# Kernel tuning notes

Hardware: AMD Instinct MI355X
Metric: run time of the kernel (lower is better)

## Reference

```python
import jax, jax.numpy as jnp
import numpy as np

N, E, C, B = 8192, 131072, 256, 64
BINS = 256
CENTERS = jnp.linspace(-6.0, 0.0, BINS)
GAMMA = 255.0 / 6.0  # 1/lengthscale, lengthscale = mean diff of centers = 6/255


def _silu(x):
    return x * jax.nn.sigmoid(x)


def _ln(x, g, b):
    m = x.mean(-1, keepdims=True)
    v = ((x - m) ** 2).mean(-1, keepdims=True)
    return (x - m) / jnp.sqrt(v + 1e-5) * g + b


def _bn(x, g, b):  # training-mode BatchNorm1d (biased var over batch dim)
    m = x.mean(0)
    v = ((x - m) ** 2).mean(0)
    return (x - m) / jnp.sqrt(v + 1e-5) * g + b


def setup_inputs() -> dict:
    key = jax.random.key(0)
    ks = list(jax.random.split(key, 60))
    it = iter(ks)

    def nrm(shape, s=0.05):
        return (jax.random.normal(next(it), shape, dtype=jnp.float32) * s)

    inp = {}
    inp['node'] = jax.random.normal(next(it), (N, 92), dtype=jnp.float32)
    inp['edge_index'] = jax.random.randint(next(it), (2, E), 0, N)
    inp['edge_attr'] = jax.random.normal(next(it), (E, 3), dtype=jnp.float32)
    inp['pdd'] = jax.random.normal(next(it), (N, 51), dtype=jnp.float32)
    inp['batch'] = jnp.sort(jax.random.randint(next(it), (N,), 0, B))
    # atom embedding: Linear(92,C) -> SiLU -> Linear(C,C)
    inp['atom_W1'] = nrm((92, C)); inp['atom_b1'] = jnp.zeros((C,), jnp.float32)
    inp['atom_W2'] = nrm((C, C)); inp['atom_b2'] = jnp.zeros((C,), jnp.float32)
    # edge embedding: RBF(256) -> Linear(256,C) -> SiLU
    inp['edge_W'] = nrm((BINS, C)); inp['edge_b'] = jnp.zeros((C,), jnp.float32)
    # pdd embedding: Linear(51,C)
    inp['pdd_W'] = nrm((51, C)); inp['pdd_b'] = jnp.zeros((C,), jnp.float32)
    # 3 PDDFormerConv layers (Matformer-style), stacked on leading dim
    inp['conv_Wq'] = nrm((3, C, C)); inp['conv_bq'] = jnp.zeros((3, C), jnp.float32)
    inp['conv_Wk'] = nrm((3, C, C)); inp['conv_bk'] = jnp.zeros((3, C), jnp.float32)
    inp['conv_Wv'] = nrm((3, C, C)); inp['conv_bv'] = jnp.zeros((3, C), jnp.float32)
    inp['conv_We'] = nrm((3, C, C)); inp['conv_be'] = jnp.zeros((3, C), jnp.float32)
    inp['conv_Wku'] = nrm((3, 3 * C, C)); inp['conv_bku'] = jnp.zeros((3, C), jnp.float32)
    inp['conv_Wmu'] = nrm((3, 3 * C, C)); inp['conv_bmu'] = jnp.zeros((3, C), jnp.float32)
    inp['conv_Wm'] = nrm((3, C, C)); inp['conv_bm'] = jnp.zeros((3, C), jnp.float32)
    inp['conv_ln_m_g'] = jnp.ones((3, C), jnp.float32); inp['conv_ln_m_b'] = jnp.zeros((3, C), jnp.float32)
    inp['conv_ln_a_g'] = jnp.ones((3, C), jnp.float32); inp['conv_ln_a_b'] = jnp.zeros((3, C), jnp.float32)
    inp['conv_bn_g'] = jnp.ones((3, C), jnp.float32); inp['conv_bn_b'] = jnp.zeros((3, C), jnp.float32)
    # 2 PDD_Conv layers
    inp['pddc_W1'] = nrm((2, C, 2 * C)); inp['pddc_b1'] = jnp.zeros((2, 2 * C), jnp.float32)
    inp['pddc_W2'] = nrm((2, C, C)); inp['pddc_b2'] = jnp.zeros((2, C), jnp.float32)
    inp['pddc_W3'] = nrm((2, C, C)); inp['pddc_b3'] = jnp.zeros((2, C), jnp.float32)
    inp['pddc_bn_g'] = jnp.ones((2, C), jnp.float32); inp['pddc_bn_b'] = jnp.zeros((2, C), jnp.float32)
    # head
    inp['fc_W'] = nrm((C, C)); inp['fc_b'] = jnp.zeros((C,), jnp.float32)
    inp['out_W'] = nrm((C, 1)); inp['out_b'] = jnp.zeros((1,), jnp.float32)
    return inp


def reference(node, edge_index, edge_attr, pdd, batch,
              atom_W1, atom_b1, atom_W2, atom_b2, edge_W, edge_b, pdd_W, pdd_b,
              conv_Wq, conv_bq, conv_Wk, conv_bk, conv_Wv, conv_bv, conv_We, conv_be,
              conv_Wku, conv_bku, conv_Wmu, conv_bmu, conv_Wm, conv_bm,
              conv_ln_m_g, conv_ln_m_b, conv_ln_a_g, conv_ln_a_b, conv_bn_g, conv_bn_b,
              pddc_W1, pddc_b1, pddc_W2, pddc_b2, pddc_W3, pddc_b3, pddc_bn_g, pddc_bn_b,
              fc_W, fc_b, out_W, out_b):
    src, dst = edge_index[0], edge_index[1]
    # embeddings
    x = _silu(node @ atom_W1 + atom_b1) @ atom_W2 + atom_b2            # [N,C]
    d = -1.0 / jnp.linalg.norm(edge_attr, axis=1)                      # [E]
    rbf = jnp.exp(-GAMMA * (d[:, None] - CENTERS) ** 2)                # [E,BINS]
    e_in = _silu(rbf @ edge_W + edge_b)                                # [E,C]
    p = pdd @ pdd_W + pdd_b                                            # [N,C]
    scale = 1.0 / jnp.sqrt(jnp.float32(C))

    def conv(x, i):
        q = x @ conv_Wq[i] + conv_bq[i]
        k = x @ conv_Wk[i] + conv_bk[i]
        v = x @ conv_Wv[i] + conv_bv[i]
        e = e_in @ conv_We[i] + conv_be[i]
        key_e = jnp.concatenate([k[dst], k[src], e], axis=-1) @ conv_Wku[i] + conv_bku[i]
        alpha = q[dst] * key_e * scale
        msg = jnp.concatenate([v[dst], v[src], e], axis=-1) @ conv_Wmu[i] + conv_bmu[i]
        msg = msg * jax.nn.sigmoid(_ln(alpha, conv_ln_a_g[i], conv_ln_a_b[i]))
        msg = _ln(msg @ conv_Wm[i] + conv_bm[i], conv_ln_m_g[i], conv_ln_m_b[i])
        agg = jax.ops.segment_sum(msg, dst, num_segments=N)
        return jax.nn.softplus(x + _bn(agg, conv_bn_g[i], conv_bn_b[i]))

    def pddc(x, adj, i):
        adj = adj + x
        a2 = _bn(adj, pddc_bn_g[i], pddc_bn_b[i]) @ pddc_W1[i] + pddc_b1[i]
        x1, x2 = a2[:, :C], a2[:, C:]
        x1 = x1 @ pddc_W2[i] + pddc_b2[i]
        x2 = jax.nn.gelu(x2, approximate=False)  # dropout inactive at eval
        return (x1 * x2) @ pddc_W3[i] + pddc_b3[i] + x, adj

    x = conv(x, 0)
    x, p = pddc(x, p, 0)
    x = conv(x, 1)
    x, p = pddc(x, p, 1)
    x = conv(x, 2)
    counts = jnp.maximum(jax.ops.segment_sum(jnp.ones((N,), x.dtype), batch, num_segments=B), 1.0)
    pooled = jax.ops.segment_sum(x, batch, num_segments=B) / counts[:, None]
    cf = pooled + _silu(pooled @ fc_W + fc_b)
    return jnp.squeeze(cf @ out_W + out_b)  # [B]
```

## Files before the change

kernel.cpp:

```cpp
#include <hip/hip_runtime.h>
#include <hip/hip_bf16.h>

#define Nn 8192
#define Ne 131072
#define Cc 256
#define Bb 64

typedef __hip_bfloat16 bf16;
typedef __attribute__((ext_vector_type(8))) short bf16x8;
typedef __attribute__((ext_vector_type(4))) float f32x4;

__device__ __forceinline__ float b2f(unsigned short s){
  return __uint_as_float(((unsigned)s) << 16);
}
__device__ __forceinline__ unsigned short f2b(float v){
  bf16 h = __float2bfloat16(v);
  return *(unsigned short*)&h;
}

__device__ __forceinline__ void block_reduce_2(float& s1, float& s2, float* sm){
#pragma unroll
  for (int off = 32; off > 0; off >>= 1){
    s1 += __shfl_down(s1, off, 64);
    s2 += __shfl_down(s2, off, 64);
  }
  int lane = threadIdx.x & 63;
  int wid  = threadIdx.x >> 6;
  if (lane == 0){ sm[wid] = s1; sm[4 + wid] = s2; }
  __syncthreads();
  s1 = sm[0] + sm[1] + sm[2] + sm[3];
  s2 = sm[4] + sm[5] + sm[6] + sm[7];
}

__global__ __launch_bounds__(256) void mg_k(
  const bf16* __restrict__ A,
  const bf16* __restrict__ Bpack, const float* __restrict__ bias,
  bf16* __restrict__ o0, bf16* __restrict__ o1, bf16* __restrict__ o2,
  bf16* __restrict__ o3, bf16* __restrict__ o4,
  float* __restrict__ fout, bf16* __restrict__ foutBf,
  int actMode, const int* __restrict__ outPerm)
{
  int lane = threadIdx.x & 63;
  int wave = threadIdx.x >> 6;
  int panel = blockIdx.x;
  long m0 = (long)blockIdx.y * 64;
  int row16 = lane & 15;
  int kg    = lane >> 4;

  const bf16* a0 = A + (m0 + row16) * 256 + kg * 8;
  const bf16* bp = Bpack + (size_t)panel * 65536;

  f32x4 acc[4][4];
#pragma unroll
  for (int i = 0; i < 4; i++)
#pragma unroll
    for (int j = 0; j < 4; j++) acc[i][j] = (f32x4){0.f, 0.f, 0.f, 0.f};

#pragma unroll
  for (int c8 = 0; c8 < 8; c8++){
    bf16x8 a[4], b[4];
#pragma unroll
    for (int im = 0; im < 4; im++)
      a[im] = *(const bf16x8*)(a0 + im * 4096 + c8 * 32);
#pragma unroll
    for (int in = 0; in < 4; in++)
      b[in] = *(const bf16x8*)(bp + ((size_t)((c8 * 16 + wave * 4 + in) * 64 + lane)) * 8);
#pragma unroll
    for (int im = 0; im < 4; im++)
#pragma unroll
      for (int in = 0; in < 4; in++)
        acc[im][in] = __builtin_amdgcn_mfma_f32_16x16x32_bf16(
                        a[im], b[in], acc[im][in], 0, 0, 0);
  }

  int colq = lane & 15;
  int quad = lane >> 4;

  if (fout){
#pragma unroll
    for (int im = 0; im < 4; im++)
#pragma unroll
      for (int in = 0; in < 4; in++){
        int col = wave * 64 + in * 16 + colq;
        float bv = bias ? bias[col] : 0.f;
#pragma unroll
        for (int r = 0; r < 4; r++){
          long row = m0 + im * 16 + quad * 4 + r;
          float v = acc[im][in][r] + bv + fout[row * 256 + col];
          fout[row * 256 + col] = v;
          if (foutBf) foutBf[row * 256 + col] = __float2bfloat16(v);
        }
      }
    return;
  }

  bf16* op = (panel == 0) ? o0 : (panel == 1) ? o1 : (panel == 2) ? o2
           : (panel == 3) ? o3 : o4;
#pragma unroll
  for (int im = 0; im < 4; im++){
    long orow[4];
#pragma unroll
    for (int r = 0; r < 4; r++){
      long row = m0 + im * 16 + quad * 4 + r;
      orow[r] = outPerm ? (long)outPerm[row] : row;
    }
#pragma unroll
    for (int in = 0; in < 4; in++){
      int col = wave * 64 + in * 16 + colq;
      float bv = bias ? bias[panel * 256 + col] : 0.f;
#pragma unroll
      for (int r = 0; r < 4; r++){
        float v = acc[im][in][r] + bv;
        if (actMode == 1) v = v / (1.f + __expf(-v));
        op[orow[r] * 256 + col] = __float2bfloat16(v);
      }
    }
  }
}

__global__ __launch_bounds__(256) void conv_edge_k(
  const bf16* __restrict__ e_in,
  const bf16* __restrict__ Bedge, const float* __restrict__ bedge,
  const bf16* __restrict__ Bm, const float* __restrict__ bm,
  const bf16* __restrict__ q,
  const bf16* __restrict__ kp1, const bf16* __restrict__ kp2,
  const bf16* __restrict__ vp1, const bf16* __restrict__ vp2,
  const int* __restrict__ dstS, const int* __restrict__ srcS,
  const float* __restrict__ lg, const float* __restrict__ lb,
  float* __restrict__ aggS)
{
  __shared__ bf16 eK[32 * 256];
  __shared__ bf16 eM[32 * 256];
  __shared__ int  sdst[32];
  int lane = threadIdx.x & 63;
  int wave = threadIdx.x >> 6;
  long m0 = (long)blockIdx.x * 32;
  int row16 = lane & 15;
  int kg    = lane >> 4;
  int colq  = row16;
  int quad  = kg;

  if (threadIdx.x < 32) sdst[threadIdx.x] = dstS[m0 + threadIdx.x];

  int drs[8], srs[8];
#pragma unroll
  for (int it = 0; it < 8; it++){
    drs[it] = dstS[m0 + it * 4 + wave];
    srs[it] = srcS[m0 + it * 4 + wave];
  }
  int c0g = lane * 4;
  ushort4 k1 = *(const ushort4*)((const unsigned short*)kp1 + (long)drs[0] * 256 + c0g);
  ushort4 k2 = *(const ushort4*)((const unsigned short*)kp2 + (long)srs[0] * 256 + c0g);
  ushort4 qv = *(const ushort4*)((const unsigned short*)q   + (long)drs[0] * 256 + c0g);
  ushort4 v1 = *(const ushort4*)((const unsigned short*)vp1 + (long)drs[0] * 256 + c0g);
  ushort4 v2 = *(const ushort4*)((const unsigned short*)vp2 + (long)srs[0] * 256 + c0g);

  const bf16* a0 = e_in + (m0 + row16) * 256 + kg * 8;

  for (int p = 0; p < 2; p++){
    const bf16* bp = Bedge + (size_t)p * 65536;
    f32x4 acc[2][4];
#pragma unroll
    for (int i = 0; i < 2; i++)
#pragma unroll
      for (int j = 0; j < 4; j++) acc[i][j] = (f32x4){0.f, 0.f, 0.f, 0.f};
#pragma unroll
    for (int c8 = 0; c8 < 8; c8++){
      bf16x8 a[2], b[4];
#pragma unroll
      for (int im = 0; im < 2; im++)
        a[im] = *(const bf16x8*)(a0 + im * 4096 + c8 * 32);
#pragma unroll
      for (int in = 0; in < 4; in++)
        b[in] = *(const bf16x8*)(bp + ((size_t)((c8 * 16 + wave * 4 + in) * 64 + lane)) * 8);
#pragma unroll
      for (int im = 0; im < 2; im++)
#pragma unroll
        for (int in = 0; in < 4; in++)
          acc[im][in] = __builtin_amdgcn_mfma_f32_16x16x32_bf16(
                          a[im], b[in], acc[im][in], 0, 0, 0);
    }
    bf16* E = p ? eM : eK;
    const float* bb = bedge + p * 256;
#pragma unroll
    for (int im = 0; im < 2; im++)
#pragma unroll
      for (int in = 0; in < 4; in++){
        int col = wave * 64 + in * 16 + colq;
        float bv = bb[col];
#pragma unroll
        for (int r = 0; r < 4; r++){
          int row = im * 16 + quad * 4 + r;
          int idx = row * 256 + ((((col >> 3) ^ (row & 7))) << 3) + (col & 7);
          E[idx] = __float2bfloat16(acc[im][in][r] + bv);
        }
      }
  }
  __syncthreads();

  {
    int cb = lane >> 1;
    int e0 = (lane & 1) * 4;
    float4 gv = *(const float4*)(lg + c0g);
    float4 bv = *(const float4*)(lb + c0g);
#pragma unroll
    for (int it = 0; it < 8; it++){
      int row = it * 4 + wave;
      int li = row * 256 + ((cb ^ (row & 7)) << 3) + e0;
      ushort4 ek = *(const ushort4*)((const unsigned short*)eK + li);
      ushort4 em = *(const ushort4*)((const unsigned short*)eM + li);
      ushort4 nk1, nk2, nqv, nv1, nv2;
      if (it < 7){
        long dr2 = drs[it + 1], sr2 = srs[it + 1];
        nk1 = *(const ushort4*)((const unsigned short*)kp1 + dr2 * 256 + c0g);
        nk2 = *(const ushort4*)((const unsigned short*)kp2 + sr2 * 256 + c0g);
        nqv = *(const ushort4*)((const unsigned short*)q   + dr2 * 256 + c0g);
        nv1 = *(const ushort4*)((const unsigned short*)vp1 + dr2 * 256 + c0g);
        nv2 = *(const ushort4*)((const unsigned short*)vp2 + sr2 * 256 + c0g);
      }
      float a0g = (b2f(ek.x) + b2f(k1.x) + b2f(k2.x)) * b2f(qv.x) * 0.0625f;
      float a1g = (b2f(ek.y) + b2f(k1.y) + b2f(k2.y)) * b2f(qv.y) * 0.0625f;
      float a2g = (b2f(ek.z) + b2f(k1.z) + b2f(k2.z)) * b2f(qv.z) * 0.0625f;
      float a3g = (b2f(ek.w) + b2f(k1.w) + b2f(k2.w)) * b2f(qv.w) * 0.0625f;
      float s1 = a0g + a1g + a2g + a3g;
      float s2 = a0g*a0g + a1g*a1g + a2g*a2g + a3g*a3g;
#pragma unroll
      for (int off = 1; off < 64; off <<= 1){
        s1 += __shfl_xor(s1, off, 64);
        s2 += __shfl_xor(s2, off, 64);
      }
      float mn  = s1 * (1.0f / Cc);
      float var = s2 * (1.0f / Cc) - mn * mn;
      float rs  = rsqrtf(var + 1e-5f);
      float g0 = 1.f / (1.f + __expf(-((a0g - mn) * rs * gv.x + bv.x)));
      float g1 = 1.f / (1.f + __expf(-((a1g - mn) * rs * gv.y + bv.y)));
      float g2 = 1.f / (1.f + __expf(-((a2g - mn) * rs * gv.z + bv.z)));
      float g3 = 1.f / (1.f + __expf(-((a3g - mn) * rs * gv.w + bv.w)));
      ushort4 o;
      o.x = f2b((b2f(em.x) + b2f(v1.x) + b2f(v2.x)) * g0);
      o.y = f2b((b2f(em.y) + b2f(v1.y) + b2f(v2.y)) * g1);
      o.z = f2b((b2f(em.z) + b2f(v1.z) + b2f(v2.z)) * g2);
      o.w = f2b((b2f(em.w) + b2f(v1.w) + b2f(v2.w)) * g3);
      *(ushort4*)((unsigned short*)eK + li) = o;
      k1 = nk1; k2 = nk2; qv = nqv; v1 = nv1; v2 = nv2;
    }
  }
  __syncthreads();

  f32x4 acc[2][4];
#pragma unroll
  for (int i = 0; i < 2; i++)
#pragma unroll
    for (int j = 0; j < 4; j++) acc[i][j] = (f32x4){0.f, 0.f, 0.f, 0.f};
  int r7 = row16 & 7;
#pragma unroll
  for (int c8 = 0; c8 < 8; c8++){
    bf16x8 a[2], b[4];
#pragma unroll
    for (int im = 0; im < 2; im++)
      a[im] = *(const bf16x8*)&eK[(row16 + im * 16) * 256 + (((c8 * 4 + kg) ^ r7) << 3)];
#pragma unroll
    for (int in = 0; in < 4; in++)
      b[in] = *(const bf16x8*)(Bm + ((size_t)((c8 * 16 + wave * 4 + in) * 64 + lane)) * 8);
#pragma unroll
    for (int im = 0; im < 2; im++)
#pragma unroll
      for (int in = 0; in < 4; in++)
        acc[im][in] = __builtin_amdgcn_mfma_f32_16x16x32_bf16(
                        a[im], b[in], acc[im][in], 0, 0, 0);
  }

  float s1a[2][4], s2a[2][4];
#pragma unroll
  for (int im = 0; im < 2; im++)
#pragma unroll
    for (int r = 0; r < 4; r++){
      float t1 = 0.f, t2 = 0.f;
#pragma unroll
      for (int in = 0; in < 4; in++){
        int col = wave * 64 + in * 16 + colq;
        float v = acc[im][in][r] + bm[col];
        t1 += v; t2 += v * v;
      }
#pragma unroll
      for (int off = 1; off < 16; off <<= 1){
        t1 += __shfl_xor(t1, off, 64);
        t2 += __shfl_xor(t2, off, 64);
      }
      s1a[im][r] = t1; s2a[im][r] = t2;
    }
  __syncthreads();
  float* red = (float*)eK;
  if (colq < 8){
    int imw = colq >> 2, rw = colq & 3;
    int rr = imw * 16 + quad * 4 + rw;
    red[(wave * 32 + rr) * 2 + 0] = s1a[imw][rw];
    red[(wave * 32 + rr) * 2 + 1] = s2a[imw][rw];
  }
  __syncthreads();
#pragma unroll
  for (int im = 0; im < 2; im++)
#pragma unroll
    for (int r = 0; r < 4; r++){
      int row = im * 16 + quad * 4 + r;
      float ts1 = red[row * 2]           + red[(32 + row) * 2]
                + red[(64 + row) * 2]    + red[(96 + row) * 2];
      float ts2 = red[row * 2 + 1]       + red[(32 + row) * 2 + 1]
                + red[(64 + row) * 2 + 1] + red[(96 + row) * 2 + 1];
      float mn  = ts1 * (1.0f / Cc);
      float var = ts2 * (1.0f / Cc) - mn * mn;
      float rs  = rsqrtf(var + 1e-5f);
#pragma unroll
      for (int in = 0; in < 4; in++){
        int col = wave * 64 + in * 16 + colq;
        float v = acc[im][in][r] + bm[col];
        ((unsigned short*)eM)[row * 256 + col] = f2b((v - mn) * rs);
      }
    }
  __syncthreads();

  {
    int t = threadIdx.x;
    float sum = 0.f;
    int cur = sdst[0];
    for (int r = 0; r < 32; r++){
      int d = sdst[r];
      if (d != cur){
        atomicAdd(&aggS[(long)cur * 256 + t], sum);
        sum = 0.f; cur = d;
      }
      sum += b2f(((const unsigned short*)eM)[r * 256 + t]);
    }
    atomicAdd(&aggS[(long)cur * 256 + t], sum);
  }
}

__global__ __launch_bounds__(256) void pack_b2_k(
  const float* __restrict__ W, int ldW, bf16* __restrict__ out)
{
  int panel = blockIdx.y;
  long p = (long)blockIdx.x * 256 + threadIdx.x;
  int j    = p & 7;
  int lane = (p >> 3) & 63;
  int nt   = (p >> 9) & 15;
  int kc   = p >> 13;
  int k = kc * 32 + (lane >> 4) * 8 + j;
  int n = nt * 16 + (lane & 15);
  out[(size_t)panel * 65536 + p] =
    __float2bfloat16(W[(long)k * ldW + panel * 256 + n]);
}

__global__ __launch_bounds__(256) void pack_qm_k(
  const float* __restrict__ Wq, const float* __restrict__ Wm,
  bf16* __restrict__ N5, bf16* __restrict__ WpM)
{
  int z = blockIdx.y;
  const float* W; bf16* out;
  if (z < 3){ W = Wq + (size_t)z * 65536; out = N5 + (size_t)z * 327680; }
  else      { W = Wm + (size_t)(z-3) * 65536; out = WpM + (size_t)(z-3) * 65536; }
  long p = (long)blockIdx.x * 256 + threadIdx.x;
  int j    = p & 7;
  int lane = (p >> 3) & 63;
  int nt   = (p >> 9) & 15;
  int kc   = p >> 13;
  int k = kc * 32 + (lane >> 4) * 8 + j;
  int n = nt * 16 + (lane & 15);
  out[p] = __float2bfloat16(W[(long)k * 256 + n]);
}

__global__ __launch_bounds__(256) void fold_k(
  const float* __restrict__ Wk, const float* __restrict__ Wv,
  const float* __restrict__ We,
  const float* __restrict__ Wku, const float* __restrict__ Wmu,
  bf16* __restrict__ N5, bf16* __restrict__ EG)
{
  int z = blockIdx.z, i = z / 6, j = z % 6;
  const float* A; const float* B; bf16* C;
  if (j < 2){
    A = Wk + (size_t)i * 65536; B = Wku + (size_t)i * 196608 + j * 65536;
    C = N5 + (size_t)i * 327680 + (size_t)(1 + j) * 65536;
  } else if (j < 4){
    A = Wv + (size_t)i * 65536; B = Wmu + (size_t)i * 196608 + (j - 2) * 65536;
    C = N5 + (size_t)i * 327680 + (size_t)(3 + (j - 2)) * 65536;
  } else {
    A = We + (size_t)i * 65536;
    B = (j == 4 ? Wku : Wmu) + (size_t)i * 196608 + 131072;
    C = EG + (size_t)i * 131072 + (size_t)(j - 4) * 65536;
  }

  __shared__ __align__(16) float As[16][64];
  __shared__ __align__(16) float Bs[16][128];
  int t = threadIdx.x;
  int m0 = blockIdx.x * 64;
  int n0 = blockIdx.y * 128;

  float acc[4][8];
#pragma unroll
  for (int a = 0; a < 4; a++)
#pragma unroll
    for (int b = 0; b < 8; b++) acc[a][b] = 0.f;
  int tm = t >> 4, tn = t & 15, mA = t & 63, kgA = t >> 6;

  for (int k0 = 0; k0 < 256; k0 += 16){
#pragma unroll
    for (int it = 0; it < 4; it++){
      int kl = kgA + it * 4;
      As[kl][mA] = A[(long)(m0 + mA) * 256 + k0 + kl];
    }
#pragma unroll
    for (int it = 0; it < 8; it++){
      int idx = t + it * 256;
      int kl = idx >> 7, n = idx & 127;
      Bs[kl][n] = B[(long)(k0 + kl) * 256 + n0 + n];
    }
    __syncthreads();
#pragma unroll
    for (int kk = 0; kk < 16; kk++){
      float4 a  = *(const float4*)&As[kk][tm * 4];
      float4 b0 = *(const float4*)&Bs[kk][tn * 4];
      float4 b1 = *(const float4*)&Bs[kk][64 + tn * 4];
      float av[4] = {a.x, a.y, a.z, a.w};
      float bv[8] = {b0.x, b0.y, b0.z, b0.w, b1.x, b1.y, b1.z, b1.w};
#pragma unroll
      for (int ii = 0; ii < 4; ii++)
#pragma unroll
        for (int jj = 0; jj < 8; jj++)
          acc[ii][jj] = __builtin_fmaf(av[ii], bv[jj], acc[ii][jj]);
    }
    __syncthreads();
  }
#pragma unroll
  for (int ii = 0; ii < 4; ii++){
    int m = m0 + tm * 4 + ii;
#pragma unroll
    for (int h = 0; h < 2; h++){
#pragma unroll
      for (int jj = 0; jj < 4; jj++){
        int n = n0 + h * 64 + tn * 4 + jj;
        int kc = m >> 5, nt = n >> 4;
        int ln_ = ((m >> 3) & 3) * 16 + (n & 15);
        long idx = ((long)(kc * 16 + nt) * 64 + ln_) * 8 + (m & 7);
        C[idx] = __float2bfloat16(acc[ii][h * 4 + jj]);
      }
    }
  }
}

__global__ __launch_bounds__(256) void gemm_k(
  const void* __restrict__ A0, int K0, int ld0,
  long M, int Nout,
  const float* __restrict__ W, const float* __restrict__ bias,
  const float* __restrict__ res, int ldRes,
  void* __restrict__ Cout, int outDt, int actMode)
{
  __shared__ __align__(16) float As[16][64];
  __shared__ __align__(16) float Bs[16][128];

  int t = threadIdx.x;
  long m0 = (long)blockIdx.x * 64;
  int  n0 = blockIdx.y * 128;

  float acc[4][8];
#pragma unroll
  for (int i = 0; i < 4; i++)
#pragma unroll
    for (int j = 0; j < 8; j++) acc[i][j] = 0.f;

  int tm = t >> 4, tn = t & 15, mA = t & 63, kgA = t >> 6;
  long rowA = m0 + mA;
  bool rv = rowA < M;

  for (int k0 = 0; k0 < K0; k0 += 16){
#pragma unroll
    for (int it = 0; it < 4; it++){
      int kl = kgA + it * 4;
      int k  = k0 + kl;
      float v = 0.f;
      if (rv && k < K0) v = ((const float*)A0)[rowA * (long)ld0 + k];
      As[kl][mA] = v;
    }
#pragma unroll
    for (int it = 0; it < 8; it++){
      int idx = t + it * 256;
      int kl = idx >> 7, n = idx & 127;
      int k  = k0 + kl;
      Bs[kl][n] = (k < K0) ? W[(long)k * Nout + n0 + n] : 0.f;
    }
    __syncthreads();
#pragma unroll
    for (int kk = 0; kk < 16; kk++){
      float4 a  = *(const float4*)&As[kk][tm * 4];
      float4 b0 = *(const float4*)&Bs[kk][tn * 4];
      float4 b1 = *(const float4*)&Bs[kk][64 + tn * 4];
      float av[4] = {a.x, a.y, a.z, a.w};
      float bv[8] = {b0.x, b0.y, b0.z, b0.w, b1.x, b1.y, b1.z, b1.w};
#pragma unroll
      for (int i = 0; i < 4; i++)
#pragma unroll
        for (int j = 0; j < 8; j++)
          acc[i][j] = __builtin_fmaf(av[i], bv[j], acc[i][j]);
    }
    __syncthreads();
  }

#pragma unroll
  for (int i = 0; i < 4; i++){
    long m = m0 + tm * 4 + i;
    if (m >= M) continue;
#pragma unroll
    for (int h = 0; h < 2; h++){
      int nb = n0 + h * 64 + tn * 4;
      float po[4];
#pragma unroll
      for (int j = 0; j < 4; j++){
        float v = acc[i][h * 4 + j];
        if (bias) v += bias[nb + j];
        if (actMode == 1) v = v / (1.0f + __expf(-v));
        if (res) v += res[m * (long)ldRes + nb + j];
        po[j] = v;
      }
      if (outDt){
        __align__(8) unsigned short tb[4];
#pragma unroll
        for (int j = 0; j < 4; j++) tb[j] = f2b(po[j]);
        *(short4*)((bf16*)Cout + m * (long)Nout + nb) = *(short4*)tb;
      } else {
        float4 ov = {po[0], po[1], po[2], po[3]};
        *(float4*)((float*)Cout + m * (long)Nout + nb) = ov;
      }
    }
  }
}

__global__ __launch_bounds__(256) void zero_k(float* __restrict__ p, long n){
  long i = (long)blockIdx.x * 256 + threadIdx.x;
  long stride = (long)gridDim.x * 256;
  for (; i < n; i += stride) p[i] = 0.f;
}
__global__ __launch_bounds__(256) void zero_i_k(int* __restrict__ p, long n){
  long i = (long)blockIdx.x * 256 + threadIdx.x;
  long stride = (long)gridDim.x * 256;
  for (; i < n; i += stride) p[i] = 0;
}
__global__ __launch_bounds__(256) void f2bf_k(bf16* __restrict__ d,
                                              const float* __restrict__ s, long n){
  long i = (long)blockIdx.x * 256 + threadIdx.x;
  long stride = (long)gridDim.x * 256;
  for (; i < n; i += stride) d[i] = __float2bfloat16(s[i]);
}

__global__ __launch_bounds__(256) void fuse_bias_all_k(
  const float* __restrict__ bku, const float* __restrict__ bmu,
  const float* __restrict__ be,
  const float* __restrict__ bk, const float* __restrict__ bv,
  const float* __restrict__ Wku, const float* __restrict__ Wmu,
  float* __restrict__ b_edge)
{
  int z = blockIdx.x, i = z >> 1, kind = z & 1;
  const float* W  = (kind ? Wmu : Wku) + (size_t)i * 196608;
  const float* b0 = (kind ? bmu : bku) + i * 256;
  const float* vb = (kind ? bv : bk) + i * 256;
  const float* eb = be + i * 256;
  int n = threadIdx.x;
  float s = b0[n];
  for (int k = 0; k < Cc; k++){
    s += eb[k] * W[(512 + k) * 256 + n];
    s += vb[k] * (W[k * 256 + n] + W[(256 + k) * 256 + n]);
  }
  b_edge[i * 512 + kind * 256 + n] = s;
}

__global__ __launch_bounds__(256) void nodeb_all_k(const float* __restrict__ bq,
                                                   float* __restrict__ out){
  int z = blockIdx.x, i = z / 5, p = z % 5;
  out[i * 1280 + p * 256 + threadIdx.x] = (p == 0) ? bq[i * 256 + threadIdx.x] : 0.f;
}

__global__ __launch_bounds__(256) void d_k(const float* __restrict__ ea,
                                           float* __restrict__ d, int E)
{
  int i = blockIdx.x * 256 + threadIdx.x;
  if (i < E){
    float a = ea[i * 3 + 0], b = ea[i * 3 + 1], c = ea[i * 3 + 2];
    d[i] = -rsqrtf(a * a + b * b + c * c);
  }
}

__global__ __launch_bounds__(256) void rbf_k(
  const float* __restrict__ d, bf16* __restrict__ out)
{
  long id = (long)blockIdx.x * 256 + threadIdx.x;
  long m = id >> 8;
  int  k = id & 255;
  float cen = -6.0f + (float)k * (6.0f / 255.0f);
  float df  = d[m] - cen;
  out[id] = __float2bfloat16(__expf(-42.5f * df * df));
}

__global__ __launch_bounds__(256) void hist_k(const int* __restrict__ dst,
                                              int* __restrict__ hist)
{
  int e = blockIdx.x * 256 + threadIdx.x;
  if (e < Ne) atomicAdd(&hist[dst[e]], 1);
}

__global__ __launch_bounds__(1024) void scan_k(
  const int* __restrict__ hist, int* __restrict__ rowptr, int* __restrict__ counter)
{
  __shared__ int part[1024];
  int t = threadIdx.x;
  int base = t * 8;
  int local[8];
  int s = 0;
#pragma unroll
  for (int i = 0; i < 8; i++){ local[i] = s; s += hist[base + i]; }
  part[t] = s;
  __syncthreads();
  for (int off = 1; off < 1024; off <<= 1){
    int v = (t >= off) ? part[t - off] : 0;
    __syncthreads();
    part[t] += v;
    __syncthreads();
  }
  int pre = (t == 0) ? 0 : part[t - 1];
#pragma unroll
  for (int i = 0; i < 8; i++){
    int rp = pre + local[i];
    rowptr[base + i] = rp;
    counter[base + i] = rp;
  }
  if (t == 1023) rowptr[8192] = part[1023];
}

__global__ __launch_bounds__(256) void perm_k(const int* __restrict__ dst,
                                              int* __restrict__ counter,
                                              int* __restrict__ pos)
{
  int e = blockIdx.x * 256 + threadIdx.x;
  if (e < Ne) pos[e] = atomicAdd(&counter[dst[e]], 1);
}

__global__ __launch_bounds__(256) void sortidx_k(
  const int* __restrict__ dst, const int* __restrict__ srcI,
  const int* __restrict__ pos, int* __restrict__ dstS, int* __restrict__ srcS)
{
  int e = blockIdx.x * 256 + threadIdx.x;
  if (e < Ne){
    int p = pos[e];
    dstS[p] = dst[e];
    srcS[p] = srcI[e];
  }
}

__global__ __launch_bounds__(256) void bn_stats_f(
  const float* __restrict__ S, const int* __restrict__ rowptr,
  const float* __restrict__ lg, const float* __restrict__ lb,
  float* __restrict__ sums)
{
  int c  = threadIdx.x;
  int r0 = blockIdx.x * 128;
  float gc = lg[c], bc = lb[c];
  float s1 = 0.f, s2 = 0.f;
  for (int r = r0; r < r0 + 128; r++){
    float cnt = (float)(rowptr[r + 1] - rowptr[r]);
    float y = gc * S[(long)r * Cc + c] + cnt * bc;
    s1 += y; s2 += y * y;
  }
  atomicAdd(&sums[c],      s1);
  atomicAdd(&sums[Cc + c], s2);
}

__global__ __launch_bounds__(256) void bn_apply_softplus_f(
  float* __restrict__ x, bf16* __restrict__ xbf,
  const float* __restrict__ S, const int* __restrict__ rowptr,
  const float* __restrict__ lg, const float* __restrict__ lb,
  const float* __restrict__ sums,
  const float* __restrict__ g, const float* __restrict__ b)
{
  long r = blockIdx.x;
  int c = threadIdx.x;
  float cnt = (float)(rowptr[r + 1] - rowptr[r]);
  float y = lg[c] * S[r * Cc + c] + cnt * lb[c];
  float m    = sums[c] * (1.0f / Nn);
  float var  = sums[Cc + c] * (1.0f / Nn) - m * m;
  float rstd = rsqrtf(var + 1e-5f);
  float bn = (y - m) * rstd * g[c] + b[c];
  float v  = x[r * Cc + c] + bn;
  float sp = (v > 0.f) ? v + log1pf(__expf(-v)) : log1pf(__expf(v));
  x[r * Cc + c] = sp;
  xbf[r * Cc + c] = __float2bfloat16(sp);
}

__global__ __launch_bounds__(256) void bn_stats_k(
  const float* __restrict__ X, int rows, float* __restrict__ sums)
{
  int c  = threadIdx.x;
  int r0 = blockIdx.x * 128;
  int re = r0 + 128; if (re > rows) re = rows;
  float s1 = 0.f, s2 = 0.f;
  for (int r = r0; r < re; r++){
    float v = X[(long)r * Cc + c];
    s1 += v; s2 += v * v;
  }
  atomicAdd(&sums[c],      s1);
  atomicAdd(&sums[Cc + c], s2);
}

__global__ __launch_bounds__(256) void bn_st_k(
  const float* __restrict__ sums, const float* __restrict__ g,
  const float* __restrict__ b, float* __restrict__ S, float* __restrict__ T)
{
  int c = threadIdx.x;
  float m    = sums[c] * (1.0f / Nn);
  float var  = sums[Cc + c] * (1.0f / Nn) - m * m;
  float rstd = rsqrtf(var + 1e-5f);
  S[c] = g[c] * rstd;
  T[c] = b[c] - m * rstd * g[c];
}

__global__ __launch_bounds__(256) void add_k(float* __restrict__ p,
                                             const float* __restrict__ x)
{
  long i = (long)blockIdx.x * 256 + threadIdx.x;
  p[i] += x[i];
}

__global__ __launch_bounds__(256) void bnaff_k(
  const float* __restrict__ p, const float* __restrict__ S,
  const float* __restrict__ T, bf16* __restrict__ out)
{
  long r = blockIdx.x;
  int c = threadIdx.x;
  out[r * 256 + c] = __float2bfloat16(p[r * 256 + c] * S[c] + T[c]);
}

__global__ __launch_bounds__(256) void mulgelu_bf_k(
  bf16* __restrict__ u, const bf16* __restrict__ x1,
  const bf16* __restrict__ a2b)
{
  long r = blockIdx.x;
  int c = threadIdx.x;
  float xg = b2f(*((const unsigned short*)a2b + r * 256 + c));
  float ge = 0.5f * xg * (1.0f + erff(xg * 0.70710678118654752f));
  float x1v = b2f(*((const unsigned short*)x1 + r * 256 + c));
  u[r * 256 + c] = __float2bfloat16(x1v * ge);
}

__global__ __launch_bounds__(256) void pool_k(
  const float* __restrict__ x, const int* __restrict__ batch,
  float* __restrict__ pooled, float* __restrict__ counts)
{
  long r = blockIdx.x;
  int c = threadIdx.x;
  long b = batch[r];
  atomicAdd(&pooled[b * Cc + c], x[r * Cc + c]);
  if (c == 0) atomicAdd(&counts[b], 1.0f);
}

__global__ __launch_bounds__(256) void pooldiv_k(
  float* __restrict__ pooled, const float* __restrict__ counts)
{
  int b = blockIdx.x;
  int c = threadIdx.x;
  float cnt = counts[b];
  if (cnt < 1.f) cnt = 1.f;
  pooled[b * Cc + c] /= cnt;
}

__global__ __launch_bounds__(256) void out_k(
  const float* __restrict__ cf, const float* __restrict__ ow,
  const float* __restrict__ ob, float* __restrict__ out)
{
  __shared__ float sm[8];
  int b = blockIdx.x;
  int c = threadIdx.x;
  float v = cf[(long)b * Cc + c] * ow[c];
  float dummy = 0.f;
  block_reduce_2(v, dummy, sm);
  if (c == 0) out[b] = v + ob[0];
}

static inline void launch_gemm(hipStream_t st,
  const void* A0, int K0, int ld0,
  long M, int Nout, const float* W, const float* bias,
  const float* res, int ldRes, void* Cout, int outDt, int act)
{
  dim3 grid((unsigned)((M + 63) / 64), (unsigned)(Nout / 128));
  gemm_k<<<grid, dim3(256), 0, st>>>(
    A0, K0, ld0, M, Nout, W, bias, res, ldRes, Cout, outDt, act);
}

static inline void launch_mg(hipStream_t st, long M, int panels,
  const bf16* A, const bf16* Bpack, const float* bias,
  bf16* o0, bf16* o1, bf16* o2, bf16* o3, bf16* o4,
  float* fout, bf16* foutBf, int act, const int* outPerm)
{
  dim3 grid((unsigned)panels, (unsigned)(M / 64));
  mg_k<<<grid, dim3(256), 0, st>>>(A, Bpack, bias, o0, o1, o2, o3, o4,
                                   fout, foutBf, act, outPerm);
}

extern "C" void kernel_launch(void* const* d_in, const int* in_sizes, int n_in,
                              void* d_out, int out_size, void* d_ws, size_t ws_size,
                              hipStream_t stream)
{
  (void)in_sizes; (void)n_in; (void)out_size; (void)ws_size;

  const float* node       = (const float*)d_in[0];
  const int*   edge_index = (const int*)  d_in[1];
  const float* edge_attr  = (const float*)d_in[2];
  const float* pdd        = (const float*)d_in[3];
  const int*   batch      = (const int*)  d_in[4];
  const float* atom_W1 = (const float*)d_in[5];
  const float* atom_b1 = (const float*)d_in[6];
  const float* atom_W2 = (const float*)d_in[7];
  const float* atom_b2 = (const float*)d_in[8];
  const float* edge_W  = (const float*)d_in[9];
  const float* edge_b  = (const float*)d_in[10];
  const float* pdd_W   = (const float*)d_in[11];
  const float* pdd_b   = (const float*)d_in[12];
  const float* conv_Wq = (const float*)d_in[13];
  const float* conv_bq = (const float*)d_in[14];
  const float* conv_Wk = (const float*)d_in[15];
  const float* conv_bk = (const float*)d_in[16];
  const float* conv_Wv = (const float*)d_in[17];
  const float* conv_bv = (const float*)d_in[18];
  const float* conv_We = (const float*)d_in[19];
  const float* conv_be = (const float*)d_in[20];
  const float* conv_Wku = (const float*)d_in[21];
  const float* conv_bku = (const float*)d_in[22];
  const float* conv_Wmu = (const float*)d_in[23];
  const float* conv_bmu = (const float*)d_in[24];
  const float* conv_Wm  = (const float*)d_in[25];
  const float* conv_bm  = (const float*)d_in[26];
  const float* ln_m_g = (const float*)d_in[27];
  const float* ln_m_b = (const float*)d_in[28];
  const float* ln_a_g = (const float*)d_in[29];
  const float* ln_a_b = (const float*)d_in[30];
  const float* bn_g   = (const float*)d_in[31];
  const float* bn_b   = (const float*)d_in[32];
  const float* pddc_W1 = (const float*)d_in[33];
  const float* pddc_b1 = (const float*)d_in[34];
  const float* pddc_W2 = (const float*)d_in[35];
  const float* pddc_b2 = (const float*)d_in[36];
  const float* pddc_W3 = (const float*)d_in[37];
  const float* pddc_b3 = (const float*)d_in[38];
  const float* pddc_bn_g = (const float*)d_in[39];
  const float* pddc_bn_b = (const float*)d_in[40];
  const float* fc_W  = (const float*)d_in[41];
  const float* fc_b  = (const float*)d_in[42];
  const float* out_W = (const float*)d_in[43];
  const float* out_b = (const float*)d_in[44];

  const int* src = edge_index;
  const int* dst = edge_index + Ne;

  char* ws = (char*)d_ws;
  size_t off = 0;
  auto alloc = [&](size_t nbytes) -> char* {
    char* ptr = ws + off;
    off += (nbytes + 255) & ~(size_t)255;
    return ptr;
  };
  bf16*  e_in = (bf16*) alloc((size_t)Ne * Cc * 2);
  bf16*  bufB = (bf16*) alloc((size_t)Ne * Cc * 2);
  bf16*  bufC = (bf16*) alloc((size_t)Ne * Cc * 2);
  float* x    = (float*)alloc((size_t)Nn * Cc * 4);
  float* p    = (float*)alloc((size_t)Nn * Cc * 4);
  float* agg  = (float*)alloc((size_t)Nn * Cc * 4);
  bf16*  x_bf  = (bf16*)alloc((size_t)Nn * Cc * 2);
  bf16*  q_bf  = (bf16*)alloc((size_t)Nn * Cc * 2);
  bf16*  kp1   = (bf16*)alloc((size_t)Nn * Cc * 2);
  bf16*  kp2   = (bf16*)alloc((size_t)Nn * Cc * 2);
  bf16*  vp1   = (bf16*)alloc((size_t)Nn * Cc * 2);
  bf16*  vp2   = (bf16*)alloc((size_t)Nn * Cc * 2);
  bf16*  WpN5  = (bf16*)alloc((size_t)3 * 5 * 65536 * 2);
  bf16*  WpEdge= (bf16*)alloc((size_t)3 * 2 * 65536 * 2);
  bf16*  WpM   = (bf16*)alloc((size_t)3 * 65536 * 2);
  bf16*  WpE   = (bf16*)alloc((size_t)65536 * 2);
  bf16*  WpP1  = (bf16*)alloc((size_t)2 * 2 * 65536 * 2);
  bf16*  WpP2  = (bf16*)alloc((size_t)2 * 65536 * 2);
  bf16*  WpP3  = (bf16*)alloc((size_t)2 * 65536 * 2);
  float* nodeb = (float*)alloc((size_t)3 * 1280 * 4);
  float* b_edge= (float*)alloc((size_t)3 * 512 * 4);
  int*   hist    = (int*)alloc((size_t)8192 * 4);
  int*   rowptr  = (int*)alloc((size_t)8193 * 4);
  int*   counter = (int*)alloc((size_t)8192 * 4);
  int*   pos     = (int*)alloc((size_t)Ne * 4);
  int*   dstS    = (int*)alloc((size_t)Ne * 4);
  int*   srcS    = (int*)alloc((size_t)Ne * 4);
  float* pooled = (float*)alloc((size_t)Bb * Cc * 4);
  float* counts = (float*)alloc((size_t)Bb * 4);
  float* cf     = (float*)alloc((size_t)Bb * Cc * 4);
  float* bnsum  = (float*)alloc(2 * Cc * 4);
  float* bnS    = (float*)alloc(Cc * 4);
  float* bnT    = (float*)alloc(Cc * 4);

  float* dArr   = (float*)bufC;
  float* hidden = (float*)(bufC + (size_t)1024 * 1024);
  bf16* a2a = bufC;
  bf16* a2b = bufC + (size_t)Nn * Cc;
  bf16* x1b = bufB;
  bf16* ub  = bufB + (size_t)Nn * Cc;

  zero_i_k<<<dim3(8), dim3(256), 0, stream>>>(hist, 8192);
  hist_k<<<dim3(Ne / 256), dim3(256), 0, stream>>>(dst, hist);
  scan_k<<<dim3(1), dim3(1024), 0, stream>>>(hist, rowptr, counter);
  perm_k<<<dim3(Ne / 256), dim3(256), 0, stream>>>(dst, counter, pos);
  sortidx_k<<<dim3(Ne / 256), dim3(256), 0, stream>>>(dst, src, pos, dstS, srcS);

  d_k<<<dim3((Ne + 255) / 256), dim3(256), 0, stream>>>(edge_attr, dArr, Ne);

  fold_k<<<dim3(4, 2, 18), dim3(256), 0, stream>>>(
    conv_Wk, conv_Wv, conv_We, conv_Wku, conv_Wmu, WpN5, WpEdge);
  pack_qm_k<<<dim3(256, 6), dim3(256), 0, stream>>>(conv_Wq, conv_Wm, WpN5, WpM);
  fuse_bias_all_k<<<dim3(6), dim3(256), 0, stream>>>(
    conv_bku, conv_bmu, conv_be, conv_bk, conv_bv, conv_Wku, conv_Wmu, b_edge);
  nodeb_all_k<<<dim3(15), dim3(256), 0, stream>>>(conv_bq, nodeb);
  pack_b2_k<<<dim3(256, 1), dim3(256), 0, stream>>>(edge_W, 256, WpE);
  for (int j = 0; j < 2; j++){
    pack_b2_k<<<dim3(256, 2), dim3(256), 0, stream>>>(
      pddc_W1 + (size_t)j * 256 * 512, 512, WpP1 + (size_t)j * 2 * 65536);
    pack_b2_k<<<dim3(256, 1), dim3(256), 0, stream>>>(
      pddc_W2 + (size_t)j * 65536, 256, WpP2 + (size_t)j * 65536);
    pack_b2_k<<<dim3(256, 1), dim3(256), 0, stream>>>(
      pddc_W3 + (size_t)j * 65536, 256, WpP3 + (size_t)j * 65536);
  }

  launch_gemm(stream, node, 92, 92, Nn, Cc, atom_W1, atom_b1,
              nullptr, 0, hidden, 0, 1);
  launch_gemm(stream, hidden, 256, 256, Nn, Cc, atom_W2, atom_b2,
              nullptr, 0, x, 0, 0);
  f2bf_k<<<dim3(512), dim3(256), 0, stream>>>(x_bf, x, (long)Nn * Cc);
  launch_gemm(stream, pdd, 51, 51, Nn, Cc, pdd_W, pdd_b,
              nullptr, 0, p, 0, 0);
  rbf_k<<<dim3(Ne), dim3(256), 0, stream>>>(dArr, bufB);
  launch_mg(stream, Ne, 1, bufB, WpE, edge_b,
            e_in, nullptr, nullptr, nullptr, nullptr, nullptr, nullptr, 1, pos);

  for (int i = 0; i < 3; i++){
    launch_mg(stream, Nn, 5, x_bf, WpN5 + (size_t)i * 5 * 65536, nodeb + i * 1280,
              q_bf, kp1, kp2, vp1, vp2, nullptr, nullptr, 0, nullptr);
    zero_k<<<dim3(1024), dim3(256), 0, stream>>>(agg, (long)Nn * Cc);
    conv_edge_k<<<dim3(Ne / 32), dim3(256), 0, stream>>>(
      e_in, WpEdge + (size_t)i * 2 * 65536, b_edge + i * 512,
      WpM + (size_t)i * 65536, conv_bm + i * 256,
      q_bf, kp1, kp2, vp1, vp2, dstS, srcS,
      ln_a_g + i * 256, ln_a_b + i * 256, agg);
    zero_k<<<dim3(2), dim3(256), 0, stream>>>(bnsum, 2 * Cc);
    bn_stats_f<<<dim3(Nn / 128), dim3(256), 0, stream>>>(agg, rowptr,
              ln_m_g + i * 256, ln_m_b + i * 256, bnsum);
    bn_apply_softplus_f<<<dim3(Nn), dim3(256), 0, stream>>>(x, x_bf, agg, rowptr,
              ln_m_g + i * 256, ln_m_b + i * 256, bnsum,
              bn_g + i * 256, bn_b + i * 256);

    if (i < 2){
      int j = i;
      add_k<<<dim3(Nn * Cc / 256), dim3(256), 0, stream>>>(p, x);
      zero_k<<<dim3(2), dim3(256), 0, stream>>>(bnsum, 2 * Cc);
      bn_stats_k<<<dim3(Nn / 128), dim3(256), 0, stream>>>(p, Nn, bnsum);
      bn_st_k<<<dim3(1), dim3(256), 0, stream>>>(bnsum,
              pddc_bn_g + j * 256, pddc_bn_b + j * 256, bnS, bnT);
      bnaff_k<<<dim3(Nn), dim3(256), 0, stream>>>(p, bnS, bnT, x_bf);
      launch_mg(stream, Nn, 2, x_bf, WpP1 + (size_t)j * 2 * 65536, pddc_b1 + j * 512,
                a2a, a2b, nullptr, nullptr, nullptr, nullptr, nullptr, 0, nullptr);
      launch_mg(stream, Nn, 1, a2a, WpP2 + (size_t)j * 65536, pddc_b2 + j * 256,
                x1b, nullptr, nullptr, nullptr, nullptr, nullptr, nullptr, 0, nullptr);
      mulgelu_bf_k<<<dim3(Nn), dim3(256), 0, stream>>>(ub, x1b, a2b);
      launch_mg(stream, Nn, 1, ub, WpP3 + (size_t)j * 65536, pddc_b3 + j * 256,
                nullptr, nullptr, nullptr, nullptr, nullptr, x, x_bf, 0, nullptr);
    }
  }

  zero_k<<<dim3(64), dim3(256), 0, stream>>>(pooled, (long)Bb * Cc);
  zero_k<<<dim3(1), dim3(256), 0, stream>>>(counts, Bb);
  pool_k<<<dim3(Nn), dim3(256), 0, stream>>>(x, batch, pooled, counts);
  pooldiv_k<<<dim3(Bb), dim3(256), 0, stream>>>(pooled, counts);
  launch_gemm(stream, pooled, 256, 256, Bb, Cc, fc_W, fc_b,
              pooled, Cc, cf, 0, 1);
  out_k<<<dim3(Bb), dim3(256), 0, stream>>>(cf, out_W, out_b, (float*)d_out);
}
```

Baseline: 1.614 ms.

## Fuse RBF into edge GEMM, GELU into GEMM epilogue, and merge small kernels

Computes the RBF expansion directly in registers inside a dedicated MFMA GEMM kernel, so the 131072x256 bf16 RBF matrix is no longer written to and read back from memory. It also fuses the GELU multiply into the pddc W2 GEMM epilogue, merges the residual add with the BN statistics pass, folds the BN scale/shift computation into the affine kernel, and combines several zeroing launches. The cost is recomputing exp in the GEMM A-operand path and per-element erf in the epilogue, plus extra global reads of the aux tensor inside the GEMM.

```diff
diff --git a/kernel.cpp b/kernel.cpp
--- a/kernel.cpp
+++ b/kernel.cpp
@@ -38,7 +38,8 @@
   bf16* __restrict__ o0, bf16* __restrict__ o1, bf16* __restrict__ o2,
   bf16* __restrict__ o3, bf16* __restrict__ o4,
   float* __restrict__ fout, bf16* __restrict__ foutBf,
-  int actMode, const int* __restrict__ outPerm)
+  int actMode, const int* __restrict__ outPerm,
+  const bf16* __restrict__ gelAux)
 {
   int lane = threadIdx.x & 63;
   int wave = threadIdx.x >> 6;
@@ -110,9 +111,83 @@
       float bv = bias ? bias[panel * 256 + col] : 0.f;
 #pragma unroll
       for (int r = 0; r < 4; r++){
+        long row = m0 + im * 16 + quad * 4 + r;
         float v = acc[im][in][r] + bv;
         if (actMode == 1) v = v / (1.f + __expf(-v));
+        if (gelAux){
+          float xg = b2f(((const unsigned short*)gelAux)[row * 256 + col]);
+          v *= 0.5f * xg * (1.0f + erff(xg * 0.70710678118654752f));
+        }
         op[orow[r] * 256 + col] = __float2bfloat16(v);
+      }
+    }
+  }
+}
+
+__global__ __launch_bounds__(256) void rbf_mg_k(
+  const float* __restrict__ dArr,
+  const bf16* __restrict__ Bpack, const float* __restrict__ bias,
+  bf16* __restrict__ out, const int* __restrict__ outPerm)
+{
+  int lane = threadIdx.x & 63;
+  int wave = threadIdx.x >> 6;
+  long m0 = (long)blockIdx.x * 64;
+  int row16 = lane & 15;
+  int kg    = lane >> 4;
+
+  float dv[4];
+#pragma unroll
+  for (int im = 0; im < 4; im++) dv[im] = dArr[m0 + row16 + im * 16];
+
+  f32x4 acc[4][4];
+#pragma unroll
+  for (int i = 0; i < 4; i++)
+#pragma unroll
+    for (int j = 0; j < 4; j++) acc[i][j] = (f32x4){0.f, 0.f, 0.f, 0.f};
+
+#pragma unroll
+  for (int c8 = 0; c8 < 8; c8++){
+    bf16x8 a[4], b[4];
+#pragma unroll
+    for (int im = 0; im < 4; im++){
+#pragma unroll
+      for (int j = 0; j < 8; j++){
+        int k = c8 * 32 + kg * 8 + j;
+        float cen = -6.0f + (float)k * (6.0f / 255.0f);
+        float df  = dv[im] - cen;
+        a[im][j] = (short)f2b(__expf(-42.5f * df * df));
+      }
+    }
+#pragma unroll
+    for (int in = 0; in < 4; in++)
+      b[in] = *(const bf16x8*)(Bpack + ((size_t)((c8 * 16 + wave * 4 + in) * 64 + lane)) * 8);
+#pragma unroll
+    for (int im = 0; im < 4; im++)
+#pragma unroll
+      for (int in = 0; in < 4; in++)
+        acc[im][in] = __builtin_amdgcn_mfma_f32_16x16x32_bf16(
+                        a[im], b[in], acc[im][in], 0, 0, 0);
+  }
+
+  int colq = lane & 15;
+  int quad = lane >> 4;
+#pragma unroll
+  for (int im = 0; im < 4; im++){
+    long orow[4];
+#pragma unroll
+    for (int r = 0; r < 4; r++){
+      long row = m0 + im * 16 + quad * 4 + r;
+      orow[r] = outPerm ? (long)outPerm[row] : row;
+    }
+#pragma unroll
+    for (int in = 0; in < 4; in++){
+      int col = wave * 64 + in * 16 + colq;
+      float bv = bias[col];
+#pragma unroll
+      for (int r = 0; r < 4; r++){
+        float v = acc[im][in][r] + bv;
+        v = v / (1.f + __expf(-v));
+        out[orow[r] * 256 + col] = __float2bfloat16(v);
       }
     }
   }
@@ -537,6 +612,13 @@
   long stride = (long)gridDim.x * 256;
   for (; i < n; i += stride) p[i] = 0.f;
 }
+__global__ __launch_bounds__(256) void zero2_k(float* __restrict__ a, long na,
+                                               float* __restrict__ b2, long nb){
+  long i = (long)blockIdx.x * 256 + threadIdx.x;
+  long stride = (long)gridDim.x * 256;
+  for (long j = i; j < na; j += stride) a[j] = 0.f;
+  for (long j = i; j < nb; j += stride) b2[j] = 0.f;
+}
 __global__ __launch_bounds__(256) void zero_i_k(int* __restrict__ p, long n){
   long i = (long)blockIdx.x * 256 + threadIdx.x;
   long stride = (long)gridDim.x * 256;
@@ -584,17 +666,6 @@
     float a = ea[i * 3 + 0], b = ea[i * 3 + 1], c = ea[i * 3 + 2];
     d[i] = -rsqrtf(a * a + b * b + c * c);
   }
-}
-
-__global__ __launch_bounds__(256) void rbf_k(
-  const float* __restrict__ d, bf16* __restrict__ out)
-{
-  long id = (long)blockIdx.x * 256 + threadIdx.x;
-  long m = id >> 8;
-  int  k = id & 255;
-  float cen = -6.0f + (float)k * (6.0f / 255.0f);
-  float df  = d[m] - cen;
-  out[id] = __float2bfloat16(__expf(-42.5f * df * df));
 }
 
 __global__ __launch_bounds__(256) void hist_k(const int* __restrict__ dst,
@@ -691,59 +762,34 @@
   xbf[r * Cc + c] = __float2bfloat16(sp);
 }
 
-__global__ __launch_bounds__(256) void bn_stats_k(
-  const float* __restrict__ X, int rows, float* __restrict__ sums)
+__global__ __launch_bounds__(256) void add_stats_k(
+  float* __restrict__ p, const float* __restrict__ x, float* __restrict__ sums)
 {
   int c  = threadIdx.x;
   int r0 = blockIdx.x * 128;
-  int re = r0 + 128; if (re > rows) re = rows;
   float s1 = 0.f, s2 = 0.f;
-  for (int r = r0; r < re; r++){
-    float v = X[(long)r * Cc + c];
+  for (int r = r0; r < r0 + 128; r++){
+    float v = p[(long)r * Cc + c] + x[(long)r * Cc + c];
+    p[(long)r * Cc + c] = v;
     s1 += v; s2 += v * v;
   }
   atomicAdd(&sums[c],      s1);
   atomicAdd(&sums[Cc + c], s2);
 }
 
-__global__ __launch_bounds__(256) void bn_st_k(
-  const float* __restrict__ sums, const float* __restrict__ g,
-  const float* __restrict__ b, float* __restrict__ S, float* __restrict__ T)
-{
+__global__ __launch_bounds__(256) void bnaff_st_k(
+  const float* __restrict__ p, const float* __restrict__ sums,
+  const float* __restrict__ g, const float* __restrict__ b,
+  bf16* __restrict__ out)
+{
+  long r = blockIdx.x;
   int c = threadIdx.x;
   float m    = sums[c] * (1.0f / Nn);
   float var  = sums[Cc + c] * (1.0f / Nn) - m * m;
   float rstd = rsqrtf(var + 1e-5f);
-  S[c] = g[c] * rstd;
-  T[c] = b[c] - m * rstd * g[c];
-}
-
-__global__ __launch_bounds__(256) void add_k(float* __restrict__ p,
-                                             const float* __restrict__ x)
-{
-  long i = (long)blockIdx.x * 256 + threadIdx.x;
-  p[i] += x[i];
-}
-
-__global__ __launch_bounds__(256) void bnaff_k(
-  const float* __restrict__ p, const float* __restrict__ S,
-  const float* __restrict__ T, bf16* __restrict__ out)
-{
-  long r = blockIdx.x;
-  int c = threadIdx.x;
-  out[r * 256 + c] = __float2bfloat16(p[r * 256 + c] * S[c] + T[c]);
-}
-
-__global__ __launch_bounds__(256) void mulgelu_bf_k(
-  bf16* __restrict__ u, const bf16* __restrict__ x1,
-  const bf16* __restrict__ a2b)
-{
-  long r = blockIdx.x;
-  int c = threadIdx.x;
-  float xg = b2f(*((const unsigned short*)a2b + r * 256 + c));
-  float ge = 0.5f * xg * (1.0f + erff(xg * 0.70710678118654752f));
-  float x1v = b2f(*((const unsigned short*)x1 + r * 256 + c));
-  u[r * 256 + c] = __float2bfloat16(x1v * ge);
+  float S = g[c] * rstd;
+  float T = b[c] - m * rstd * g[c];
+  out[r * 256 + c] = __float2bfloat16(p[r * 256 + c] * S + T);
 }
 
 __global__ __launch_bounds__(256) void pool_k(
@@ -793,11 +839,12 @@
 static inline void launch_mg(hipStream_t st, long M, int panels,
   const bf16* A, const bf16* Bpack, const float* bias,
   bf16* o0, bf16* o1, bf16* o2, bf16* o3, bf16* o4,
-  float* fout, bf16* foutBf, int act, const int* outPerm)
+  float* fout, bf16* foutBf, int act, const int* outPerm,
+  const bf16* gelAux = nullptr)
 {
   dim3 grid((unsigned)panels, (unsigned)(M / 64));
   mg_k<<<grid, dim3(256), 0, st>>>(A, Bpack, bias, o0, o1, o2, o3, o4,
-                                   fout, foutBf, act, outPerm);
+                                   fout, foutBf, act, outPerm, gelAux);
 }
 
 extern "C" void kernel_launch(void* const* d_in, const int* in_sizes, int n_in,
@@ -893,15 +940,12 @@
   float* counts = (float*)alloc((size_t)Bb * 4);
   float* cf     = (float*)alloc((size_t)Bb * Cc * 4);
   float* bnsum  = (float*)alloc(2 * Cc * 4);
-  float* bnS    = (float*)alloc(Cc * 4);
-  float* bnT    = (float*)alloc(Cc * 4);
 
   float* dArr   = (float*)bufC;
   float* hidden = (float*)(bufC + (size_t)1024 * 1024);
   bf16* a2a = bufC;
   bf16* a2b = bufC + (size_t)Nn * Cc;
-  bf16* x1b = bufB;
-  bf16* ub  = bufB + (size_t)Nn * Cc;
+  bf16* ub  = bufB;
 
   zero_i_k<<<dim3(8), dim3(256), 0, stream>>>(hist, 8192);
   hist_k<<<dim3(Ne / 256), dim3(256), 0, stream>>>(dst, hist);
@@ -934,20 +978,17 @@
   f2bf_k<<<dim3(512), dim3(256), 0, stream>>>(x_bf, x, (long)Nn * Cc);
   launch_gemm(stream, pdd, 51, 51, Nn, Cc, pdd_W, pdd_b,
               nullptr, 0, p, 0, 0);
-  rbf_k<<<dim3(Ne), dim3(256), 0, stream>>>(dArr, bufB);
-  launch_mg(stream, Ne, 1, bufB, WpE, edge_b,
-            e_in, nullptr, nullptr, nullptr, nullptr, nullptr, nullptr, 1, pos);
+  rbf_mg_k<<<dim3(Ne / 64), dim3(256), 0, stream>>>(dArr, WpE, edge_b, e_in, pos);
 
   for (int i = 0; i < 3; i++){
     launch_mg(stream, Nn, 5, x_bf, WpN5 + (size_t)i * 5 * 65536, nodeb + i * 1280,
               q_bf, kp1, kp2, vp1, vp2, nullptr, nullptr, 0, nullptr);
-    zero_k<<<dim3(1024), dim3(256), 0, stream>>>(agg, (long)Nn * Cc);
+    zero2_k<<<dim3(1024), dim3(256), 0, stream>>>(agg, (long)Nn * Cc, bnsum, 512);
     conv_edge_k<<<dim3(Ne / 32), dim3(256), 0, stream>>>(
       e_in, WpEdge + (size_t)i * 2 * 65536, b_edge + i * 512,
       WpM + (size_t)i * 65536, conv_bm + i * 256,
       q_bf, kp1, kp2, vp1, vp2, dstS, srcS,
       ln_a_g + i * 256, ln_a_b + i * 256, agg);
-    zero_k<<<dim3(2), dim3(256), 0, stream>>>(bnsum, 2 * Cc);
     bn_stats_f<<<dim3(Nn / 128), dim3(256), 0, stream>>>(agg, rowptr,
               ln_m_g + i * 256, ln_m_b + i * 256, bnsum);
     bn_apply_softplus_f<<<dim3(Nn), dim3(256), 0, stream>>>(x, x_bf, agg, rowptr,
@@ -956,24 +997,21 @@
 
     if (i < 2){
       int j = i;
-      add_k<<<dim3(Nn * Cc / 256), dim3(256), 0, stream>>>(p, x);
       zero_k<<<dim3(2), dim3(256), 0, stream>>>(bnsum, 2 * Cc);
-      bn_stats_k<<<dim3(Nn / 128), dim3(256), 0, stream>>>(p, Nn, bnsum);
-      bn_st_k<<<dim3(1), dim3(256), 0, stream>>>(bnsum,
-              pddc_bn_g + j * 256, pddc_bn_b + j * 256, bnS, bnT);
-      bnaff_k<<<dim3(Nn), dim3(256), 0, stream>>>(p, bnS, bnT, x_bf);
+      add_stats_k<<<dim3(Nn / 128), dim3(256), 0, stream>>>(p, x, bnsum);
+      bnaff_st_k<<<dim3(Nn), dim3(256), 0, stream>>>(p, bnsum,
+              pddc_bn_g + j * 256, pddc_bn_b + j * 256, x_bf);
       launch_mg(stream, Nn, 2, x_bf, WpP1 + (size_t)j * 2 * 65536, pddc_b1 + j * 512,
                 a2a, a2b, nullptr, nullptr, nullptr, nullptr, nullptr, 0, nullptr);
       launch_mg(stream, Nn, 1, a2a, WpP2 + (size_t)j * 65536, pddc_b2 + j * 256,
-                x1b, nullptr, nullptr, nullptr, nullptr, nullptr, nullptr, 0, nullptr);
-      mulgelu_bf_k<<<dim3(Nn), dim3(256), 0, stream>>>(ub, x1b, a2b);
+                ub, nullptr, nullptr, nullptr, nullptr, nullptr, nullptr, 0, nullptr,
+                a2b);
       launch_mg(stream, Nn, 1, ub, WpP3 + (size_t)j * 65536, pddc_b3 + j * 256,
                 nullptr, nullptr, nullptr, nullptr, nullptr, x, x_bf, 0, nullptr);
     }
   }
 
-  zero_k<<<dim3(64), dim3(256), 0, stream>>>(pooled, (long)Bb * Cc);
-  zero_k<<<dim3(1), dim3(256), 0, stream>>>(counts, Bb);
+  zero2_k<<<dim3(64), dim3(256), 0, stream>>>(pooled, (long)Bb * Cc, counts, Bb);
   pool_k<<<dim3(Nn), dim3(256), 0, stream>>>(x, batch, pooled, counts);
   pooldiv_k<<<dim3(Bb), dim3(256), 0, stream>>>(pooled, counts);
   launch_gemm(stream, pooled, 256, 256, Bb, Cc, fc_W, fc_b,
```

Result: faster. 1.527 ms (-5.4%).
